# Kernel optimization log

Hardware: AMD Instinct MI355X
Metric: run time of the kernel (lower is better)

Reference implementation:

```python
import jax, jax.numpy as jnp
import numpy as np

N = 10000        # num_nodes
F_IN = 256       # dataset_num_features
H = 128          # hidden_channels
C_OUT = 40       # dataset_num_classes
L = 3            # num_layers
HEADS = 8
DH = H // HEADS  # per-head dim
E = 160000       # num edges (before self loops)
SCALE = 1.0 / float(np.sqrt(DH))


def setup_inputs() -> dict:
    key = jax.random.key(0)
    ks = jax.random.split(key, 8)
    s = lambda k, *sh: (jax.random.normal(k, sh, dtype=jnp.float32) * 0.05)
    return dict(
        edge_index=jax.random.randint(ks[0], (2, E), 0, N, dtype=jnp.int32),
        x_param=s(ks[1], N, F_IN),
        lin1_w=s(ks[2], F_IN, H),
        lin1_b=jnp.zeros((H,), jnp.float32),
        wq=s(ks[3], L, H, H),
        wk=s(ks[4], L, H, H),
        wv=s(ks[5], L, H, H),
        bq=jnp.zeros((L, H), jnp.float32),
        bk=jnp.zeros((L, H), jnp.float32),
        bv=jnp.zeros((L, H), jnp.float32),
        lin2_w=s(ks[6], H, C_OUT),
        lin2_b=jnp.zeros((C_OUT,), jnp.float32),
    )


def _gcn_norm(edge_index):
    # PyG gcn_norm: add self loops (weight 1), symmetric D^-1/2 A D^-1/2
    loops = jnp.arange(N, dtype=edge_index.dtype)
    row = jnp.concatenate([edge_index[0], loops])  # source j
    col = jnp.concatenate([edge_index[1], loops])  # target i
    deg = jax.ops.segment_sum(jnp.ones(row.shape, jnp.float32), col, num_segments=N)
    dis = jnp.where(deg > 0, jax.lax.rsqrt(jnp.maximum(deg, 1e-12)), 0.0)
    return row, col, dis[row] * dis[col]


def _restricted_softmax(score):
    # softmax with an implicit extra logit at `margin=0`
    m = jnp.maximum(jnp.max(score, axis=-1, keepdims=True), 0.0)
    e = jnp.exp(score - m)
    return e / (jnp.sum(e, axis=-1, keepdims=True) + jnp.exp(-m))


def _forward(edge_index, x_param, lin1_w, lin1_b, wq, wk, wv, bq, bk, bv, lin2_w, lin2_b):
    row, col, norm = _gcn_norm(edge_index)
    # dropouts are eval-mode no-ops
    x = jax.nn.relu(x_param @ lin1_w + lin1_b)  # [N, H]
    x_all = x[:, None, :]                       # [N, 1, H]
    for l in range(L):
        t = x_all.shape[1]
        # project per-node first (linear commutes with per-edge gather)
        q = (x_all[:, -1] @ wq[l] + bq[l]).reshape(N, HEADS, DH)      # query from latest state
        k = (x_all @ wk[l] + bk[l]).reshape(N, t, HEADS, DH)          # keys over full history
        v = (x_all @ wv[l] + bv[l]).reshape(N, t, HEADS, DH)
        qe = q[col]   # [Etot, heads, dh]   (x_i)
        ke = k[row]   # [Etot, t, heads, dh] (x_j)
        ve = v[row]
        score = jnp.einsum('ehd,ethd->eht', qe, ke) * SCALE
        attn = _restricted_softmax(score)        # attention-dropout is a no-op in eval
        msg = jnp.einsum('eht,ethd->ehd', attn, ve).reshape(-1, H) * norm[:, None]
        out = jax.ops.segment_sum(msg, col, num_segments=N)  # aggr='add'
        x = jax.nn.relu(out)
        x_all = jnp.concatenate([x_all, x[:, None, :]], axis=1)
    logits = x_all[:, -1] @ lin2_w + lin2_b
    return jax.nn.log_softmax(logits, axis=1)


def reference(edge_index, x_param, lin1_w, lin1_b, wq, wk, wv, bq, bk, bv, lin2_w, lin2_b):
    return _forward(edge_index, x_param, lin1_w, lin1_b, wq, wk, wv, bq, bk, bv, lin2_w, lin2_b)
```

## Files before the change

### kernel.cpp

```cpp
#include <hip/hip_runtime.h>
#include <math.h>

#define N_NODES 10000
#define F_IN_D  256
#define H_DIM   128
#define C_OUTD  40
#define NHEADS  8
#define NEDGES  160000
#define ETOT    (NEDGES + N_NODES)
#define SCALE_F 0.25f
#define TILES_N 157
#define KVSZ    ((size_t)N_NODES * 3 * 256)

typedef __attribute__((ext_vector_type(8))) short bf16x8;
typedef __attribute__((ext_vector_type(4))) float f32x4;
typedef __attribute__((ext_vector_type(2))) float f32x2;

__device__ __forceinline__ unsigned short f2bf(float f) {
    unsigned int u = __float_as_uint(f);
    unsigned int r = (u + 0x7FFFu + ((u >> 16) & 1u)) >> 16;
    return (unsigned short)r;
}
__device__ __forceinline__ float bf2f(unsigned short h) {
    return __uint_as_float(((unsigned int)h) << 16);
}
__device__ __forceinline__ unsigned char f2fp8(float v) {
    int pk = __builtin_amdgcn_cvt_pk_fp8_f32(v, v, 0, false);
    return (unsigned char)(pk & 0xff);
}


__global__ __launch_bounds__(256) void k_prep1(const float* __restrict__ w1,
                                               unsigned short* __restrict__ W1T,
                                               int* __restrict__ degi) {
    int t = blockIdx.x * 256 + threadIdx.x;
    if (t < 8192) {
        float4 v = *(const float4*)(w1 + 4 * t);
        int e = 4 * t;
        #pragma unroll
        for (int i = 0; i < 4; ++i) {
            int k = (e + i) >> 7, n = (e + i) & 127;
            W1T[n * 256 + k] = f2bf(((const float*)&v)[i]);
        }
    } else if (t < 10692) {
        int idx = (t - 8192) * 4;
        *(int4*)&degi[idx] = make_int4(0, 0, 0, 0);
    }
}


__device__ __forceinline__ void lin1_block(int bid, int ct0, const float* __restrict__ X,
                                           const unsigned short* __restrict__ W1T,
                                           const float* __restrict__ b1,
                                           unsigned short* __restrict__ X0, int nct) {
    int tid = threadIdx.x;
    int wid = tid >> 6, lane = tid & 63;
    int m = lane & 15, quad = lane >> 4;
    int rowA = bid * 64 + wid * 16 + m;
    int rowc = rowA < N_NODES ? rowA : N_NODES - 1;
    bf16x8 af[8];
    const float* ap = X + (size_t)rowc * F_IN_D + quad * 8;
    #pragma unroll
    for (int s = 0; s < 8; ++s) {
        float4 lo = *(const float4*)(ap + s * 32);
        float4 hi = *(const float4*)(ap + s * 32 + 4);
        union { unsigned short u[8]; bf16x8 v; } pk;
        pk.u[0] = f2bf(lo.x); pk.u[1] = f2bf(lo.y);
        pk.u[2] = f2bf(lo.z); pk.u[3] = f2bf(lo.w);
        pk.u[4] = f2bf(hi.x); pk.u[5] = f2bf(hi.y);
        pk.u[6] = f2bf(hi.z); pk.u[7] = f2bf(hi.w);
        af[s] = pk.v;
    }
    int row0 = bid * 64 + wid * 16 + quad * 4;
    for (int ct = ct0; ct < ct0 + nct; ++ct) {
        int col = ct * 16 + m;
        const unsigned short* bp = W1T + (size_t)col * F_IN_D + quad * 8;
        f32x4 acc = {0.f, 0.f, 0.f, 0.f};
        #pragma unroll
        for (int s = 0; s < 8; ++s) {
            bf16x8 bfr = __builtin_bit_cast(bf16x8, *(const uint4*)(bp + s * 32));
            acc = __builtin_amdgcn_mfma_f32_16x16x32_bf16(af[s], bfr, acc, 0, 0, 0);
        }
        float bb = b1[col];
        #pragma unroll
        for (int rg = 0; rg < 4; ++rg) {
            int r = row0 + rg;
            if (r < N_NODES)
                X0[(size_t)r * H_DIM + col] = f2bf(fmaxf(acc[rg] + bb, 0.f));
        }
    }
}

__device__ __forceinline__ void qkv_block(int mi, int rt,
                                          const unsigned short* __restrict__ XHb,
                                          const unsigned short* __restrict__ WTq_l,
                                          const unsigned short* __restrict__ WTk_l,
                                          const unsigned short* __restrict__ WTv_l,
                                          const float* __restrict__ bq_l,
                                          const float* __restrict__ bk_l,
                                          const float* __restrict__ bv_l,
                                          unsigned short* __restrict__ Qb,
                                          unsigned char* __restrict__ KVb,
                                          int hasQ, int qslice, int nK, int sbase,
                                          int cp0, int nct) {
    int tid = threadIdx.x;
    int wid = tid >> 6, lane = tid & 63;
    int m = lane & 15, quad = lane >> 4;
    const unsigned short* WT; const float* bias; int slice, mode;
    if (hasQ && mi == 0) { WT = WTq_l; bias = bq_l; slice = qslice; mode = 0; }
    else {
        int j = mi - hasQ;
        if (j < nK) { WT = WTk_l; bias = bk_l; slice = sbase + j;      mode = 1; }
        else        { WT = WTv_l; bias = bv_l; slice = sbase + j - nK; mode = 2; }
    }
    const unsigned short* A = XHb + (size_t)slice * N_NODES * H_DIM;
    int rowA = rt * 64 + wid * 16 + m;
    bf16x8 af[4];
    const unsigned short* ap = A + (size_t)rowA * H_DIM + quad * 8;
    #pragma unroll
    for (int s = 0; s < 4; ++s)
        af[s] = __builtin_bit_cast(bf16x8, *(const uint4*)(ap + s * 32));
    int row0 = rt * 64 + wid * 16 + quad * 4;
    int vofs = (mode == 2) ? 8 : 0;
    for (int cp = cp0; cp < cp0 + nct; ++cp) {
        int colA = cp * 32 + m;
        int colB = colA + 16;
        const unsigned short* bpA = WT + (size_t)colA * H_DIM + quad * 8;
        const unsigned short* bpB = WT + (size_t)colB * H_DIM + quad * 8;
        bf16x8 bA[4], bB[4];
        #pragma unroll
        for (int s = 0; s < 4; ++s) {
            bA[s] = __builtin_bit_cast(bf16x8, *(const uint4*)(bpA + s * 32));
            bB[s] = __builtin_bit_cast(bf16x8, *(const uint4*)(bpB + s * 32));
        }
        f32x4 accA = {0.f, 0.f, 0.f, 0.f};
        f32x4 accB = {0.f, 0.f, 0.f, 0.f};
        #pragma unroll
        for (int s = 0; s < 4; ++s) {
            accA = __builtin_amdgcn_mfma_f32_16x16x32_bf16(af[s], bA[s], accA, 0, 0, 0);
            accB = __builtin_amdgcn_mfma_f32_16x16x32_bf16(af[s], bB[s], accB, 0, 0, 0);
        }
        float bbA = bias[colA], bbB = bias[colB];
        #pragma unroll
        for (int rg = 0; rg < 4; ++rg) {
            int r = row0 + rg;
            if (r < N_NODES) {
                float vA = accA[rg] + bbA;
                float vB = accB[rg] + bbB;
                if (mode == 0) {
                    Qb[(size_t)r * H_DIM + colA] = f2bf(vA * SCALE_F);
                    Qb[(size_t)r * H_DIM + colB] = f2bf(vB * SCALE_F);
                } else {
                    size_t nb = ((size_t)r * 3 + slice) * 256;
                    KVb[nb + (colA >> 3) * 16 + (colA & 7) + vofs] = f2fp8(vA);
                    KVb[nb + (colB >> 3) * 16 + (colB & 7) + vofs] = f2fp8(vB);
                }
            }
        }
    }
}


template <int T>
__device__ __forceinline__ void kv_load(const uint4* __restrict__ KV, int r, int ci,
                                        uint4 (&kv)[T]) {
    const uint4* p = KV + (size_t)r * 48 + ci;
    #pragma unroll
    for (int s = 0; s < T; ++s) kv[s] = p[s * 16];
}

template <int T>
__device__ __forceinline__ void edge_accum(const uint4 (&kv)[T], const float (&q)[8],
                                           float nrm, float (&a)[8]) {
    float den = 1.f;
    float mv[8];
    #pragma unroll
    for (int i = 0; i < 8; ++i) mv[i] = 0.f;
    #pragma unroll
    for (int s = 0; s < T; ++s) {
        f32x2 k0 = __builtin_amdgcn_cvt_pk_f32_fp8(kv[s].x, false);
        f32x2 k1 = __builtin_amdgcn_cvt_pk_f32_fp8(kv[s].x, true);
        f32x2 k2 = __builtin_amdgcn_cvt_pk_f32_fp8(kv[s].y, false);
        f32x2 k3 = __builtin_amdgcn_cvt_pk_f32_fp8(kv[s].y, true);
        float p = q[0] * k0[0] + q[1] * k0[1] + q[2] * k1[0] + q[3] * k1[1]
                + q[4] * k2[0] + q[5] * k2[1] + q[6] * k3[0] + q[7] * k3[1];
        p += __shfl_xor(p, 1, 2);
        float w = __expf(p);
        den += w;
        f32x2 v0 = __builtin_amdgcn_cvt_pk_f32_fp8(kv[s].z, false);
        f32x2 v1 = __builtin_amdgcn_cvt_pk_f32_fp8(kv[s].z, true);
        f32x2 v2 = __builtin_amdgcn_cvt_pk_f32_fp8(kv[s].w, false);
        f32x2 v3 = __builtin_amdgcn_cvt_pk_f32_fp8(kv[s].w, true);
        mv[0] += w * v0[0]; mv[1] += w * v0[1];
        mv[2] += w * v1[0]; mv[3] += w * v1[1];
        mv[4] += w * v2[0]; mv[5] += w * v2[1];
        mv[6] += w * v3[0]; mv[7] += w * v3[1];
    }
    float ws = __fdividef(nrm, den);
    #pragma unroll
    for (int i = 0; i < 8; ++i) a[i] += ws * mv[i];
}

template <int T, bool LOGITS>
__device__ __forceinline__ void attn_block(int bid, const unsigned short* __restrict__ Q,
                                           const uint4* __restrict__ KV,
                                           const int2* __restrict__ csr,
                                           const int* __restrict__ degi,
                                           unsigned int* __restrict__ Xout,
                                           const unsigned short* __restrict__ W2T,
                                           const float* __restrict__ b2,
                                           float* __restrict__ out) {
    int tid = threadIdx.x;
    int wid = tid >> 6, lane = tid & 63;
    int quarter = lane >> 4, ci = lane & 15;
    int n = bid * 4 + wid;

    int cnt = degi[n] + 1;
    if (cnt > 64) cnt = 64;
    int li = lane < cnt ? lane : cnt - 1;
    int2 eAll = csr[(n << 6) + li];
    int   rAll = eAll.x;
    float nAll = (lane < cnt) ? __int_as_float(eAll.y) : 0.f;

    float q[8];
    {
        uint4 qp = *(const uint4*)&Q[(size_t)n * H_DIM + ci * 8];
        q[0] = __uint_as_float(qp.x << 16);
        q[1] = __uint_as_float(qp.x & 0xffff0000u);
        q[2] = __uint_as_float(qp.y << 16);
        q[3] = __uint_as_float(qp.y & 0xffff0000u);
        q[4] = __uint_as_float(qp.z << 16);
        q[5] = __uint_as_float(qp.z & 0xffff0000u);
        q[6] = __uint_as_float(qp.w << 16);
        q[7] = __uint_as_float(qp.w & 0xffff0000u);
    }
    int nq = (cnt + 3) >> 2;
    float a[8];
    #pragma unroll
    for (int i = 0; i < 8; ++i) a[i] = 0.f;

    auto rowN = [&](int j4) { return __shfl(rAll, j4 < 63 ? j4 : 63, 64); };
    auto nrmN = [&](int j4) { return __shfl(nAll, j4 < 63 ? j4 : 63, 64); };

    uint4 kv0[T], kv1[T], kv2[T], kv3[T];
    kv_load<T>(KV, rowN(quarter), ci, kv0);
    kv_load<T>(KV, rowN(4 + quarter), ci, kv1);
    kv_load<T>(KV, rowN(8 + quarter), ci, kv2);
    kv_load<T>(KV, rowN(12 + quarter), ci, kv3);

    int j = 0;
    for (;;) {
        edge_accum<T>(kv0, q, nrmN(j * 4 + quarter), a);
        if (++j >= nq) break;
        kv_load<T>(KV, rowN((j + 3) * 4 + quarter), ci, kv0);
        edge_accum<T>(kv1, q, nrmN(j * 4 + quarter), a);
        if (++j >= nq) break;
        kv_load<T>(KV, rowN((j + 3) * 4 + quarter), ci, kv1);
        edge_accum<T>(kv2, q, nrmN(j * 4 + quarter), a);
        if (++j >= nq) break;
        kv_load<T>(KV, rowN((j + 3) * 4 + quarter), ci, kv2);
        edge_accum<T>(kv3, q, nrmN(j * 4 + quarter), a);
        if (++j >= nq) break;
        kv_load<T>(KV, rowN((j + 3) * 4 + quarter), ci, kv3);
    }

    #pragma unroll
    for (int i = 0; i < 8; ++i) {
        a[i] += __shfl_xor(a[i], 16, 64);
        a[i] += __shfl_xor(a[i], 32, 64);
    }

    if (!LOGITS) {
        if (quarter == 0) {
            uint4 o;
            o.x = ((unsigned int)f2bf(fmaxf(a[1], 0.f)) << 16) | (unsigned int)f2bf(fmaxf(a[0], 0.f));
            o.y = ((unsigned int)f2bf(fmaxf(a[3], 0.f)) << 16) | (unsigned int)f2bf(fmaxf(a[2], 0.f));
            o.z = ((unsigned int)f2bf(fmaxf(a[5], 0.f)) << 16) | (unsigned int)f2bf(fmaxf(a[4], 0.f));
            o.w = ((unsigned int)f2bf(fmaxf(a[7], 0.f)) << 16) | (unsigned int)f2bf(fmaxf(a[6], 0.f));
            *(uint4*)&Xout[(size_t)n * 64 + ci * 4] = o;
        }
        return;
    }

    float x[8];
    #pragma unroll
    for (int i = 0; i < 8; ++i) x[i] = fmaxf(a[i], 0.f);
    float lg[10];
    #pragma unroll
    for (int jj = 0; jj < 10; ++jj) {
        int c = quarter * 10 + jj;
        uint4 w = *(const uint4*)&W2T[c * H_DIM + ci * 8];
        float p = x[0] * bf2f((unsigned short)(w.x & 0xffff))
                + x[1] * bf2f((unsigned short)(w.x >> 16))
                + x[2] * bf2f((unsigned short)(w.y & 0xffff))
                + x[3] * bf2f((unsigned short)(w.y >> 16))
                + x[4] * bf2f((unsigned short)(w.z & 0xffff))
                + x[5] * bf2f((unsigned short)(w.z >> 16))
                + x[6] * bf2f((unsigned short)(w.w & 0xffff))
                + x[7] * bf2f((unsigned short)(w.w >> 16));
        #pragma unroll
        for (int o = 1; o < 16; o <<= 1) p += __shfl_xor(p, o, 16);
        lg[jj] = p + b2[c];
    }
    float mx = lg[0];
    #pragma unroll
    for (int jj = 1; jj < 10; ++jj) mx = fmaxf(mx, lg[jj]);
    mx = fmaxf(mx, __shfl_xor(mx, 16, 64));
    mx = fmaxf(mx, __shfl_xor(mx, 32, 64));
    float sm = 0.f;
    #pragma unroll
    for (int jj = 0; jj < 10; ++jj) sm += __expf(lg[jj] - mx);
    sm += __shfl_xor(sm, 16, 64);
    sm += __shfl_xor(sm, 32, 64);
    float lse = mx + __logf(sm);
    if (ci == 0) {
        float* op = out + (size_t)n * C_OUTD + quarter * 10;
        #pragma unroll
        for (int jj = 0; jj < 10; ++jj) op[jj] = lg[jj] - lse;
    }
}


__global__ __launch_bounds__(256) void k_deg_lin1(const int* __restrict__ col,
                                                  int* __restrict__ degi,
                                                  int* __restrict__ slotbuf,
                                                  const float* __restrict__ X,
                                                  const unsigned short* __restrict__ W1T,
                                                  const float* __restrict__ b1,
                                                  unsigned short* __restrict__ X0,
                                                  const float* __restrict__ wq,
                                                  const float* __restrict__ wk,
                                                  const float* __restrict__ wv,
                                                  const float* __restrict__ w2,
                                                  unsigned short* __restrict__ WTq,
                                                  unsigned short* __restrict__ WTk,
                                                  unsigned short* __restrict__ WTv,
                                                  unsigned short* __restrict__ W2T,
                                                  int nct) {
    int b = blockIdx.x;
    if (b < 625) {
        int e = b * 256 + threadIdx.x;
        slotbuf[e] = atomicAdd(&degi[col[e]], 1);
        return;
    }
    if (b < 939) {
        int bid = b - 625;
        lin1_block(bid % TILES_N, (bid / TILES_N) * 4, X, W1T, b1, X0, nct);
        return;
    }
    int t = (b - 939) * 256 + threadIdx.x;
    if (t < 36864) {
        int mat = t >> 12;
        int l = mat / 3, ws = mat % 3;
        const float*    src = (ws == 0) ? wq  : (ws == 1) ? wk  : wv;
        unsigned short* dst = (ws == 0) ? WTq : (ws == 1) ? WTk : WTv;
        int e2 = (t & 4095) * 4;
        float4 v = *(const float4*)(src + l * 16384 + e2);
        #pragma unroll
        for (int i = 0; i < 4; ++i) {
            int k = (e2 + i) >> 7, n = (e2 + i) & 127;
            dst[l * 16384 + n * 128 + k] = f2bf(((const float*)&v)[i]);
        }
    } else if (t < 38144) {
        int e = (t - 36864) * 4;
        float4 v = *(const float4*)(w2 + e);
        #pragma unroll
        for (int i = 0; i < 4; ++i) {
            int ee = e + i;
            int k = ee / 40, c = ee - k * 40;
            W2T[c * H_DIM + k] = f2bf(((const float*)&v)[i]);
        }
    }
}

__global__ __launch_bounds__(256) void k_scatter_qkv0(const int* __restrict__ row,
                                                      const int* __restrict__ col,
                                                      const int* __restrict__ degi,
                                                      const int* __restrict__ slotbuf,
                                                      int2* __restrict__ csr,
                                                      const unsigned short* __restrict__ XHb,
                                                      const unsigned short* __restrict__ WTq,
                                                      const unsigned short* __restrict__ WTk,
                                                      const unsigned short* __restrict__ WTv,
                                                      const float* __restrict__ bq,
                                                      const float* __restrict__ bk,
                                                      const float* __restrict__ bv,
                                                      unsigned short* __restrict__ Qb,
                                                      unsigned char* __restrict__ KVb) {
    if (blockIdx.x < 665) {
        int e = blockIdx.x * 256 + threadIdx.x;
        if (e >= ETOT) return;
        int r, c, slot;
        if (e < NEDGES) { r = row[e]; c = col[e]; slot = slotbuf[e]; }
        else            { r = c = e - NEDGES; slot = degi[c]; }
        if (slot > 63) slot = 63;
        float dr = rsqrtf((float)(degi[r] + 1));
        float dc = rsqrtf((float)(degi[c] + 1));
        int2 ent; ent.x = r; ent.y = __float_as_int(dr * dc);
        csr[(c << 6) + slot] = ent;
        return;
    }
    int b = blockIdx.x - 665;
    int quarter = b / (3 * TILES_N);
    int bb = b % (3 * TILES_N);
    qkv_block(bb / TILES_N, bb % TILES_N, XHb, WTq, WTk, WTv, bq, bk, bv,
              Qb, KVb, 1, 0, 1, 0, quarter, 1);
}

__global__ __launch_bounds__(256) void k_attn0_old(const unsigned short* __restrict__ Q,
                                                   const uint4* __restrict__ KV,
                                                   const int2* __restrict__ csr,
                                                   const int* __restrict__ degi,
                                                   unsigned int* __restrict__ Xout,
                                                   const unsigned short* __restrict__ XHb,
                                                   const unsigned short* __restrict__ WTk,
                                                   const unsigned short* __restrict__ WTv,
                                                   const float* __restrict__ bk,
                                                   const float* __restrict__ bv,
                                                   unsigned char* __restrict__ B1,
                                                   unsigned char* __restrict__ B2) {
    if (blockIdx.x < 2500) {
        attn_block<1, false>(blockIdx.x, Q, KV, csr, degi, Xout,
                             nullptr, nullptr, nullptr);
        return;
    }
    int bb = blockIdx.x - 2500;
    int layer = bb / (2 * TILES_N);
    int r = bb % (2 * TILES_N);
    int mi = r / TILES_N;
    int rt = r % TILES_N;
    int woff = (layer + 1) * 16384;
    unsigned char* dst = layer ? B2 : B1;
    qkv_block(mi, rt, XHb, nullptr, WTk + woff, WTv + woff, nullptr,
              bk + (layer + 1) * H_DIM, bv + (layer + 1) * H_DIM, nullptr,
              dst, 0, 0, 1, 0, 0, 4);
}

__global__ __launch_bounds__(256) void k_qkvnew1_old2b(const unsigned short* __restrict__ XHb,
                                                       const unsigned short* __restrict__ WTq,
                                                       const unsigned short* __restrict__ WTk,
                                                       const unsigned short* __restrict__ WTv,
                                                       const float* __restrict__ bq,
                                                       const float* __restrict__ bk,
                                                       const float* __restrict__ bv,
                                                       unsigned short* __restrict__ Qb,
                                                       unsigned char* __restrict__ B1,
                                                       unsigned char* __restrict__ B2) {
    int b = blockIdx.x;
    if (b < 12 * TILES_N) {
        int quarter = b / (3 * TILES_N);
        int bb = b % (3 * TILES_N);
        qkv_block(bb / TILES_N, bb % TILES_N, XHb,
                  WTq + 16384, WTk + 16384, WTv + 16384,
                  bq + H_DIM, bk + H_DIM, bv + H_DIM,
                  Qb, B1, 1, 1, 1, 1, quarter, 1);
        return;
    }
    int b2 = b - 12 * TILES_N;
    int quarter = b2 / (2 * TILES_N);
    int bb = b2 % (2 * TILES_N);
    int mi = bb / TILES_N;
    qkv_block(mi, bb % TILES_N, XHb, nullptr, WTk + 32768, WTv + 32768, nullptr,
              bk + 2 * H_DIM, bv + 2 * H_DIM, nullptr,
              B2, 0, 0, 1, 1, quarter, 1);
}

template <int T>
__global__ __launch_bounds__(256) void k_attn_pure(const unsigned short* __restrict__ Q,
                                                   const uint4* __restrict__ KV,
                                                   const int2* __restrict__ csr,
                                                   const int* __restrict__ degi,
                                                   unsigned int* __restrict__ Xout) {
    attn_block<T, false>(blockIdx.x, Q, KV, csr, degi, Xout,
                         nullptr, nullptr, nullptr);
}

__global__ __launch_bounds__(256) void k_qkv2(const unsigned short* __restrict__ XHb,
                                              const unsigned short* __restrict__ WTq,
                                              const unsigned short* __restrict__ WTk,
                                              const unsigned short* __restrict__ WTv,
                                              const float* __restrict__ bq,
                                              const float* __restrict__ bk,
                                              const float* __restrict__ bv,
                                              unsigned short* __restrict__ Qb,
                                              unsigned char* __restrict__ B2) {
    int quarter = blockIdx.x / (3 * TILES_N);
    int bb = blockIdx.x % (3 * TILES_N);
    qkv_block(bb / TILES_N, bb % TILES_N, XHb,
              WTq + 32768, WTk + 32768, WTv + 32768,
              bq + 2 * H_DIM, bk + 2 * H_DIM, bv + 2 * H_DIM,
              Qb, B2, 1, 2, 1, 2, quarter, 1);
}

__global__ __launch_bounds__(256) void k_attn_logits(const unsigned short* __restrict__ Q,
                                                     const uint4* __restrict__ KV,
                                                     const int2* __restrict__ csr,
                                                     const int* __restrict__ degi,
                                                     const unsigned short* __restrict__ W2T,
                                                     const float* __restrict__ b2,
                                                     float* __restrict__ out) {
    attn_block<3, true>(blockIdx.x, Q, KV, csr, degi, nullptr, W2T, b2, out);
}


extern "C" void kernel_launch(void* const* d_in, const int* in_sizes, int n_in,
                              void* d_out, int out_size, void* d_ws, size_t ws_size,
                              hipStream_t stream) {
    const int*   ei      = (const int*)d_in[0];
    const int*   row     = ei;
    const int*   col     = ei + NEDGES;
    const float* x_param = (const float*)d_in[1];
    const float* lin1_w  = (const float*)d_in[2];
    const float* lin1_b  = (const float*)d_in[3];
    const float* wq      = (const float*)d_in[4];
    const float* wk      = (const float*)d_in[5];
    const float* wv      = (const float*)d_in[6];
    const float* bq      = (const float*)d_in[7];
    const float* bk      = (const float*)d_in[8];
    const float* bv      = (const float*)d_in[9];
    const float* lin2_w  = (const float*)d_in[10];
    const float* lin2_b  = (const float*)d_in[11];
    float*       out     = (float*)d_out;

    char* wbase = (char*)d_ws;
    size_t off = 0;
    auto alloc = [&](size_t bytes) -> void* {
        off = (off + 255) & ~(size_t)255;
        void* p = wbase + off;
        off += bytes;
        return p;
    };
    int*            degi     = (int*)           alloc((size_t)N_NODES * 4);
    int*            slotbuf  = (int*)           alloc((size_t)NEDGES * 4);
    int2*           csr      = (int2*)          alloc((size_t)N_NODES * 64 * 8);
    unsigned short* W1T      = (unsigned short*)alloc((size_t)H_DIM * F_IN_D * 2);
    unsigned short* WTq      = (unsigned short*)alloc((size_t)3 * H_DIM * H_DIM * 2);
    unsigned short* WTk      = (unsigned short*)alloc((size_t)3 * H_DIM * H_DIM * 2);
    unsigned short* WTv      = (unsigned short*)alloc((size_t)3 * H_DIM * H_DIM * 2);
    unsigned short* W2T      = (unsigned short*)alloc((size_t)C_OUTD * H_DIM * 2);
    unsigned short* XHb      = (unsigned short*)alloc((size_t)3 * N_NODES * H_DIM * 2);
    unsigned short* Qb       = (unsigned short*)alloc((size_t)N_NODES * H_DIM * 2);
    unsigned char*  KVb      = (unsigned char*) alloc(3 * KVSZ);
    unsigned char*  B0 = KVb;
    unsigned char*  B1 = KVb + KVSZ;
    unsigned char*  B2 = KVb + 2 * KVSZ;

    k_prep1<<<42, 256, 0, stream>>>(lin1_w, W1T, degi);

    k_deg_lin1<<<1089, 256, 0, stream>>>(col, degi, slotbuf,
                                         x_param, W1T, lin1_b, XHb,
                                         wq, wk, wv, lin2_w,
                                         WTq, WTk, WTv, W2T, 4);

    k_scatter_qkv0<<<665 + 12 * TILES_N, 256, 0, stream>>>(
        row, col, degi, slotbuf, csr,
        XHb, WTq, WTk, WTv, bq, bk, bv, Qb, B0);

    unsigned int* X1 = (unsigned int*)(XHb + (size_t)1 * N_NODES * H_DIM);
    unsigned int* X2 = (unsigned int*)(XHb + (size_t)2 * N_NODES * H_DIM);

    k_attn0_old<<<2500 + 4 * TILES_N, 256, 0, stream>>>(
        Qb, (const uint4*)B0, csr, degi, X1,
        XHb, WTk, WTv, bk, bv, B1, B2);

    k_qkvnew1_old2b<<<20 * TILES_N, 256, 0, stream>>>(
        XHb, WTq, WTk, WTv, bq, bk, bv, Qb, B1, B2);

    k_attn_pure<2><<<2500, 256, 0, stream>>>(Qb, (const uint4*)B1, csr, degi, X2);

    k_qkv2<<<12 * TILES_N, 256, 0, stream>>>(
        XHb, WTq, WTk, WTv, bq, bk, bv, Qb, B2);

    k_attn_logits<<<2500, 256, 0, stream>>>(Qb, (const uint4*)B2, csr, degi,
                                            W2T, lin2_b, out);
}
```

Measured before the change: 219.3 us.

## Fuse lin1 with layer-0 QKV projections via LDS and build CSR in one pass

Weight transposes are merged into a single prep kernel. lin1 output is kept in LDS and immediately projected to Q and to all K/V history slices for every layer, so X0 never goes to global memory. The CSR build now stores source ids directly through a single atomic pass, and edge norms are recomputed from degrees inside the attention kernels, which removes the slotbuf pass and halves the CSR entry size. The schedule drops from 8 launches to 7, at the cost of serial per-block projection work in the fused kernel and extra degree lookups during attention.

```diff
diff --git a/kernel.cpp b/kernel.cpp
--- a/kernel.cpp
+++ b/kernel.cpp
@@ -7,7 +7,6 @@
 #define C_OUTD  40
 #define NHEADS  8
 #define NEDGES  160000
-#define ETOT    (NEDGES + N_NODES)
 #define SCALE_F 0.25f
 #define TILES_N 157
 #define KVSZ    ((size_t)N_NODES * 3 * 256)
@@ -30,9 +29,17 @@
 }
 
 
-__global__ __launch_bounds__(256) void k_prep1(const float* __restrict__ w1,
-                                               unsigned short* __restrict__ W1T,
-                                               int* __restrict__ degi) {
+__global__ __launch_bounds__(256) void k_prep_all(const float* __restrict__ w1,
+                                                  const float* __restrict__ wq,
+                                                  const float* __restrict__ wk,
+                                                  const float* __restrict__ wv,
+                                                  const float* __restrict__ w2,
+                                                  unsigned short* __restrict__ W1T,
+                                                  unsigned short* __restrict__ WTq,
+                                                  unsigned short* __restrict__ WTk,
+                                                  unsigned short* __restrict__ WTv,
+                                                  unsigned short* __restrict__ W2T,
+                                                  int* __restrict__ degi) {
     int t = blockIdx.x * 256 + threadIdx.x;
     if (t < 8192) {
         float4 v = *(const float4*)(w1 + 4 * t);
@@ -42,86 +49,44 @@
             int k = (e + i) >> 7, n = (e + i) & 127;
             W1T[n * 256 + k] = f2bf(((const float*)&v)[i]);
         }
-    } else if (t < 10692) {
-        int idx = (t - 8192) * 4;
+    } else if (t < 45056) {
+        int u = t - 8192;
+        int mat = u >> 12;
+        int l = mat / 3, ws = mat % 3;
+        const float*    src = (ws == 0) ? wq  : (ws == 1) ? wk  : wv;
+        unsigned short* dst = (ws == 0) ? WTq : (ws == 1) ? WTk : WTv;
+        int e2 = (u & 4095) * 4;
+        float4 v = *(const float4*)(src + l * 16384 + e2);
+        #pragma unroll
+        for (int i = 0; i < 4; ++i) {
+            int k = (e2 + i) >> 7, n = (e2 + i) & 127;
+            dst[l * 16384 + n * 128 + k] = f2bf(((const float*)&v)[i]);
+        }
+    } else if (t < 46336) {
+        int e = (t - 45056) * 4;
+        float4 v = *(const float4*)(w2 + e);
+        #pragma unroll
+        for (int i = 0; i < 4; ++i) {
+            int ee = e + i;
+            int k = ee / 40, c = ee - k * 40;
+            W2T[c * H_DIM + k] = f2bf(((const float*)&v)[i]);
+        }
+    } else if (t < 48836) {
+        int idx = (t - 46336) * 4;
         *(int4*)&degi[idx] = make_int4(0, 0, 0, 0);
     }
 }
 
 
-__device__ __forceinline__ void lin1_block(int bid, int ct0, const float* __restrict__ X,
-                                           const unsigned short* __restrict__ W1T,
-                                           const float* __restrict__ b1,
-                                           unsigned short* __restrict__ X0, int nct) {
-    int tid = threadIdx.x;
-    int wid = tid >> 6, lane = tid & 63;
-    int m = lane & 15, quad = lane >> 4;
-    int rowA = bid * 64 + wid * 16 + m;
-    int rowc = rowA < N_NODES ? rowA : N_NODES - 1;
-    bf16x8 af[8];
-    const float* ap = X + (size_t)rowc * F_IN_D + quad * 8;
-    #pragma unroll
-    for (int s = 0; s < 8; ++s) {
-        float4 lo = *(const float4*)(ap + s * 32);
-        float4 hi = *(const float4*)(ap + s * 32 + 4);
-        union { unsigned short u[8]; bf16x8 v; } pk;
-        pk.u[0] = f2bf(lo.x); pk.u[1] = f2bf(lo.y);
-        pk.u[2] = f2bf(lo.z); pk.u[3] = f2bf(lo.w);
-        pk.u[4] = f2bf(hi.x); pk.u[5] = f2bf(hi.y);
-        pk.u[6] = f2bf(hi.z); pk.u[7] = f2bf(hi.w);
-        af[s] = pk.v;
-    }
-    int row0 = bid * 64 + wid * 16 + quad * 4;
-    for (int ct = ct0; ct < ct0 + nct; ++ct) {
-        int col = ct * 16 + m;
-        const unsigned short* bp = W1T + (size_t)col * F_IN_D + quad * 8;
-        f32x4 acc = {0.f, 0.f, 0.f, 0.f};
-        #pragma unroll
-        for (int s = 0; s < 8; ++s) {
-            bf16x8 bfr = __builtin_bit_cast(bf16x8, *(const uint4*)(bp + s * 32));
-            acc = __builtin_amdgcn_mfma_f32_16x16x32_bf16(af[s], bfr, acc, 0, 0, 0);
-        }
-        float bb = b1[col];
-        #pragma unroll
-        for (int rg = 0; rg < 4; ++rg) {
-            int r = row0 + rg;
-            if (r < N_NODES)
-                X0[(size_t)r * H_DIM + col] = f2bf(fmaxf(acc[rg] + bb, 0.f));
-        }
-    }
-}
-
-__device__ __forceinline__ void qkv_block(int mi, int rt,
-                                          const unsigned short* __restrict__ XHb,
-                                          const unsigned short* __restrict__ WTq_l,
-                                          const unsigned short* __restrict__ WTk_l,
-                                          const unsigned short* __restrict__ WTv_l,
-                                          const float* __restrict__ bq_l,
-                                          const float* __restrict__ bk_l,
-                                          const float* __restrict__ bv_l,
-                                          unsigned short* __restrict__ Qb,
-                                          unsigned char* __restrict__ KVb,
-                                          int hasQ, int qslice, int nK, int sbase,
-                                          int cp0, int nct) {
-    int tid = threadIdx.x;
-    int wid = tid >> 6, lane = tid & 63;
-    int m = lane & 15, quad = lane >> 4;
-    const unsigned short* WT; const float* bias; int slice, mode;
-    if (hasQ && mi == 0) { WT = WTq_l; bias = bq_l; slice = qslice; mode = 0; }
-    else {
-        int j = mi - hasQ;
-        if (j < nK) { WT = WTk_l; bias = bk_l; slice = sbase + j;      mode = 1; }
-        else        { WT = WTv_l; bias = bv_l; slice = sbase + j - nK; mode = 2; }
-    }
-    const unsigned short* A = XHb + (size_t)slice * N_NODES * H_DIM;
-    int rowA = rt * 64 + wid * 16 + m;
-    bf16x8 af[4];
-    const unsigned short* ap = A + (size_t)rowA * H_DIM + quad * 8;
-    #pragma unroll
-    for (int s = 0; s < 4; ++s)
-        af[s] = __builtin_bit_cast(bf16x8, *(const uint4*)(ap + s * 32));
-    int row0 = rt * 64 + wid * 16 + quad * 4;
+__device__ __forceinline__ void proj_frags(const bf16x8 (&af)[4], int row0, int m,
+                                           int quad,
+                                           const unsigned short* __restrict__ WT,
+                                           const float* __restrict__ bias, int mode,
+                                           unsigned short* __restrict__ Qb,
+                                           unsigned char* __restrict__ KVbuf,
+                                           int kvslice, int cp0, int nct) {
     int vofs = (mode == 2) ? 8 : 0;
+    #pragma unroll 1
     for (int cp = cp0; cp < cp0 + nct; ++cp) {
         int colA = cp * 32 + m;
         int colB = colA + 16;
@@ -151,13 +116,118 @@
                     Qb[(size_t)r * H_DIM + colA] = f2bf(vA * SCALE_F);
                     Qb[(size_t)r * H_DIM + colB] = f2bf(vB * SCALE_F);
                 } else {
-                    size_t nb = ((size_t)r * 3 + slice) * 256;
-                    KVb[nb + (colA >> 3) * 16 + (colA & 7) + vofs] = f2fp8(vA);
-                    KVb[nb + (colB >> 3) * 16 + (colB & 7) + vofs] = f2fp8(vB);
+                    size_t nb = ((size_t)r * 3 + kvslice) * 256;
+                    KVbuf[nb + (colA >> 3) * 16 + (colA & 7) + vofs] = f2fp8(vA);
+                    KVbuf[nb + (colB >> 3) * 16 + (colB & 7) + vofs] = f2fp8(vB);
                 }
             }
         }
     }
+}
+
+__device__ __forceinline__ void qkv_mat(int mode, int rt,
+                                        const unsigned short* __restrict__ A,
+                                        const unsigned short* __restrict__ WT,
+                                        const float* __restrict__ bias,
+                                        unsigned short* __restrict__ Qb,
+                                        unsigned char* __restrict__ KVbuf,
+                                        int kvslice, int cp0, int nct) {
+    int tid = threadIdx.x;
+    int wid = tid >> 6, lane = tid & 63;
+    int m = lane & 15, quad = lane >> 4;
+    int rowA = rt * 64 + wid * 16 + m;
+    bf16x8 af[4];
+    const unsigned short* ap = A + (size_t)rowA * H_DIM + quad * 8;
+    #pragma unroll
+    for (int s = 0; s < 4; ++s)
+        af[s] = __builtin_bit_cast(bf16x8, *(const uint4*)(ap + s * 32));
+    int row0 = rt * 64 + wid * 16 + quad * 4;
+    proj_frags(af, row0, m, quad, WT, bias, mode, Qb, KVbuf, kvslice, cp0, nct);
+}
+
+
+#define LDS_W 136
+
+__global__ __launch_bounds__(256) void k_fused0(const float* __restrict__ X,
+                                                const unsigned short* __restrict__ W1T,
+                                                const float* __restrict__ b1,
+                                                const int* __restrict__ erow,
+                                                const int* __restrict__ ecol,
+                                                int* __restrict__ degi,
+                                                int* __restrict__ csr,
+                                                const unsigned short* __restrict__ WTq,
+                                                const unsigned short* __restrict__ WTk,
+                                                const unsigned short* __restrict__ WTv,
+                                                const float* __restrict__ bq,
+                                                const float* __restrict__ bk,
+                                                const float* __restrict__ bv,
+                                                unsigned short* __restrict__ Qb,
+                                                unsigned char* __restrict__ B0,
+                                                unsigned char* __restrict__ B1,
+                                                unsigned char* __restrict__ B2,
+                                                int nct) {
+    __shared__ unsigned short xl[64][LDS_W];
+    if (blockIdx.x >= TILES_N) {
+        int e = (blockIdx.x - TILES_N) * 256 + threadIdx.x;
+        int c = ecol[e];
+        int slot = atomicAdd(&degi[c], 1);
+        if (slot < 64) csr[(c << 6) + slot] = erow[e];
+        return;
+    }
+    int rt = blockIdx.x;
+    int tid = threadIdx.x;
+    int wid = tid >> 6, lane = tid & 63;
+    int m = lane & 15, quad = lane >> 4;
+
+    {
+        int rowA = rt * 64 + wid * 16 + m;
+        int rowc = rowA < N_NODES ? rowA : N_NODES - 1;
+        bf16x8 af8[8];
+        const float* ap = X + (size_t)rowc * F_IN_D + quad * 8;
+        #pragma unroll
+        for (int s = 0; s < 8; ++s) {
+            float4 lo = *(const float4*)(ap + s * 32);
+            float4 hi = *(const float4*)(ap + s * 32 + 4);
+            union { unsigned short u[8]; bf16x8 v; } pk;
+            pk.u[0] = f2bf(lo.x); pk.u[1] = f2bf(lo.y);
+            pk.u[2] = f2bf(lo.z); pk.u[3] = f2bf(lo.w);
+            pk.u[4] = f2bf(hi.x); pk.u[5] = f2bf(hi.y);
+            pk.u[6] = f2bf(hi.z); pk.u[7] = f2bf(hi.w);
+            af8[s] = pk.v;
+        }
+        #pragma unroll 1
+        for (int ct = 0; ct < 2 * nct; ++ct) {
+            int col = ct * 16 + m;
+            const unsigned short* bp = W1T + (size_t)col * F_IN_D + quad * 8;
+            f32x4 acc = {0.f, 0.f, 0.f, 0.f};
+            #pragma unroll
+            for (int s = 0; s < 8; ++s) {
+                bf16x8 bfr = __builtin_bit_cast(bf16x8, *(const uint4*)(bp + s * 32));
+                acc = __builtin_amdgcn_mfma_f32_16x16x32_bf16(af8[s], bfr, acc, 0, 0, 0);
+            }
+            float bb = b1[col];
+            #pragma unroll
+            for (int rg = 0; rg < 4; ++rg)
+                xl[wid * 16 + quad * 4 + rg][col] = f2bf(fmaxf(acc[rg] + bb, 0.f));
+        }
+    }
+    __syncthreads();
+
+    bf16x8 af[4];
+    {
+        int rl = wid * 16 + m;
+        #pragma unroll
+        for (int s = 0; s < 4; ++s)
+            af[s] = *(const bf16x8*)&xl[rl][quad * 8 + s * 32];
+    }
+    int row0 = rt * 64 + wid * 16 + quad * 4;
+    proj_frags(af, row0, m, quad, WTq,         bq,             0, Qb, nullptr, 0, 0, nct);
+    proj_frags(af, row0, m, quad, WTk,         bk,             1, nullptr, B0, 0, 0, nct);
+    proj_frags(af, row0, m, quad, WTv,         bv,             2, nullptr, B0, 0, 0, nct);
+    proj_frags(af, row0, m, quad, WTk + 16384, bk + H_DIM,     1, nullptr, B1, 0, 0, nct);
+    proj_frags(af, row0, m, quad, WTv + 16384, bv + H_DIM,     2, nullptr, B1, 0, 0, nct);
+    proj_frags(af, row0, m, quad, WTk + 32768, bk + 2 * H_DIM, 1, nullptr, B2, 0, 0, nct);
+    proj_frags(af, row0, m, quad, WTv + 32768, bv + 2 * H_DIM, 2, nullptr, B2, 0, 0, nct);
 }
 
 
@@ -204,7 +274,7 @@
 template <int T, bool LOGITS>
 __device__ __forceinline__ void attn_block(int bid, const unsigned short* __restrict__ Q,
                                            const uint4* __restrict__ KV,
-                                           const int2* __restrict__ csr,
+                                           const int* __restrict__ csr,
                                            const int* __restrict__ degi,
                                            unsigned int* __restrict__ Xout,
                                            const unsigned short* __restrict__ W2T,
@@ -215,12 +285,15 @@
     int quarter = lane >> 4, ci = lane & 15;
     int n = bid * 4 + wid;
 
-    int cnt = degi[n] + 1;
+    int dn = degi[n];
+    int cnt = dn + 1;
     if (cnt > 64) cnt = 64;
-    int li = lane < cnt ? lane : cnt - 1;
-    int2 eAll = csr[(n << 6) + li];
-    int   rAll = eAll.x;
-    float nAll = (lane < cnt) ? __int_as_float(eAll.y) : 0.f;
+    float rn = rsqrtf((float)(dn + 1));
+    int csrv = csr[(n << 6) + lane];
+    int r = (lane < cnt - 1) ? csrv : n;
+    int dr = degi[r];
+    int   rAll = r;
+    float nAll = (lane < cnt) ? rsqrtf((float)(dr + 1)) * rn : 0.f;
 
     float q[8];
     {
@@ -321,161 +394,17 @@
 }
 
 
-__global__ __launch_bounds__(256) void k_deg_lin1(const int* __restrict__ col,
-                                                  int* __restrict__ degi,
-                                                  int* __restrict__ slotbuf,
-                                                  const float* __restrict__ X,
-                                                  const unsigned short* __restrict__ W1T,
-                                                  const float* __restrict__ b1,
-                                                  unsigned short* __restrict__ X0,
-                                                  const float* __restrict__ wq,
-                                                  const float* __restrict__ wk,
-                                                  const float* __restrict__ wv,
-                                                  const float* __restrict__ w2,
-                                                  unsigned short* __restrict__ WTq,
-                                                  unsigned short* __restrict__ WTk,
-                                                  unsigned short* __restrict__ WTv,
-                                                  unsigned short* __restrict__ W2T,
-                                                  int nct) {
-    int b = blockIdx.x;
-    if (b < 625) {
-        int e = b * 256 + threadIdx.x;
-        slotbuf[e] = atomicAdd(&degi[col[e]], 1);
-        return;
-    }
-    if (b < 939) {
-        int bid = b - 625;
-        lin1_block(bid % TILES_N, (bid / TILES_N) * 4, X, W1T, b1, X0, nct);
-        return;
-    }
-    int t = (b - 939) * 256 + threadIdx.x;
-    if (t < 36864) {
-        int mat = t >> 12;
-        int l = mat / 3, ws = mat % 3;
-        const float*    src = (ws == 0) ? wq  : (ws == 1) ? wk  : wv;
-        unsigned short* dst = (ws == 0) ? WTq : (ws == 1) ? WTk : WTv;
-        int e2 = (t & 4095) * 4;
-        float4 v = *(const float4*)(src + l * 16384 + e2);
-        #pragma unroll
-        for (int i = 0; i < 4; ++i) {
-            int k = (e2 + i) >> 7, n = (e2 + i) & 127;
-            dst[l * 16384 + n * 128 + k] = f2bf(((const float*)&v)[i]);
-        }
-    } else if (t < 38144) {
-        int e = (t - 36864) * 4;
-        float4 v = *(const float4*)(w2 + e);
-        #pragma unroll
-        for (int i = 0; i < 4; ++i) {
-            int ee = e + i;
-            int k = ee / 40, c = ee - k * 40;
-            W2T[c * H_DIM + k] = f2bf(((const float*)&v)[i]);
-        }
-    }
-}
-
-__global__ __launch_bounds__(256) void k_scatter_qkv0(const int* __restrict__ row,
-                                                      const int* __restrict__ col,
-                                                      const int* __restrict__ degi,
-                                                      const int* __restrict__ slotbuf,
-                                                      int2* __restrict__ csr,
-                                                      const unsigned short* __restrict__ XHb,
-                                                      const unsigned short* __restrict__ WTq,
-                                                      const unsigned short* __restrict__ WTk,
-                                                      const unsigned short* __restrict__ WTv,
-                                                      const float* __restrict__ bq,
-                                                      const float* __restrict__ bk,
-                                                      const float* __restrict__ bv,
-                                                      unsigned short* __restrict__ Qb,
-                                                      unsigned char* __restrict__ KVb) {
-    if (blockIdx.x < 665) {
-        int e = blockIdx.x * 256 + threadIdx.x;
-        if (e >= ETOT) return;
-        int r, c, slot;
-        if (e < NEDGES) { r = row[e]; c = col[e]; slot = slotbuf[e]; }
-        else            { r = c = e - NEDGES; slot = degi[c]; }
-        if (slot > 63) slot = 63;
-        float dr = rsqrtf((float)(degi[r] + 1));
-        float dc = rsqrtf((float)(degi[c] + 1));
-        int2 ent; ent.x = r; ent.y = __float_as_int(dr * dc);
-        csr[(c << 6) + slot] = ent;
-        return;
-    }
-    int b = blockIdx.x - 665;
-    int quarter = b / (3 * TILES_N);
-    int bb = b % (3 * TILES_N);
-    qkv_block(bb / TILES_N, bb % TILES_N, XHb, WTq, WTk, WTv, bq, bk, bv,
-              Qb, KVb, 1, 0, 1, 0, quarter, 1);
-}
-
-__global__ __launch_bounds__(256) void k_attn0_old(const unsigned short* __restrict__ Q,
-                                                   const uint4* __restrict__ KV,
-                                                   const int2* __restrict__ csr,
-                                                   const int* __restrict__ degi,
-                                                   unsigned int* __restrict__ Xout,
-                                                   const unsigned short* __restrict__ XHb,
-                                                   const unsigned short* __restrict__ WTk,
-                                                   const unsigned short* __restrict__ WTv,
-                                                   const float* __restrict__ bk,
-                                                   const float* __restrict__ bv,
-                                                   unsigned char* __restrict__ B1,
-                                                   unsigned char* __restrict__ B2) {
-    if (blockIdx.x < 2500) {
-        attn_block<1, false>(blockIdx.x, Q, KV, csr, degi, Xout,
-                             nullptr, nullptr, nullptr);
-        return;
-    }
-    int bb = blockIdx.x - 2500;
-    int layer = bb / (2 * TILES_N);
-    int r = bb % (2 * TILES_N);
-    int mi = r / TILES_N;
-    int rt = r % TILES_N;
-    int woff = (layer + 1) * 16384;
-    unsigned char* dst = layer ? B2 : B1;
-    qkv_block(mi, rt, XHb, nullptr, WTk + woff, WTv + woff, nullptr,
-              bk + (layer + 1) * H_DIM, bv + (layer + 1) * H_DIM, nullptr,
-              dst, 0, 0, 1, 0, 0, 4);
-}
-
-__global__ __launch_bounds__(256) void k_qkvnew1_old2b(const unsigned short* __restrict__ XHb,
-                                                       const unsigned short* __restrict__ WTq,
-                                                       const unsigned short* __restrict__ WTk,
-                                                       const unsigned short* __restrict__ WTv,
-                                                       const float* __restrict__ bq,
-                                                       const float* __restrict__ bk,
-                                                       const float* __restrict__ bv,
-                                                       unsigned short* __restrict__ Qb,
-                                                       unsigned char* __restrict__ B1,
-                                                       unsigned char* __restrict__ B2) {
-    int b = blockIdx.x;
-    if (b < 12 * TILES_N) {
-        int quarter = b / (3 * TILES_N);
-        int bb = b % (3 * TILES_N);
-        qkv_block(bb / TILES_N, bb % TILES_N, XHb,
-                  WTq + 16384, WTk + 16384, WTv + 16384,
-                  bq + H_DIM, bk + H_DIM, bv + H_DIM,
-                  Qb, B1, 1, 1, 1, 1, quarter, 1);
-        return;
-    }
-    int b2 = b - 12 * TILES_N;
-    int quarter = b2 / (2 * TILES_N);
-    int bb = b2 % (2 * TILES_N);
-    int mi = bb / TILES_N;
-    qkv_block(mi, bb % TILES_N, XHb, nullptr, WTk + 32768, WTv + 32768, nullptr,
-              bk + 2 * H_DIM, bv + 2 * H_DIM, nullptr,
-              B2, 0, 0, 1, 1, quarter, 1);
-}
-
 template <int T>
 __global__ __launch_bounds__(256) void k_attn_pure(const unsigned short* __restrict__ Q,
                                                    const uint4* __restrict__ KV,
-                                                   const int2* __restrict__ csr,
+                                                   const int* __restrict__ csr,
                                                    const int* __restrict__ degi,
                                                    unsigned int* __restrict__ Xout) {
     attn_block<T, false>(blockIdx.x, Q, KV, csr, degi, Xout,
                          nullptr, nullptr, nullptr);
 }
 
-__global__ __launch_bounds__(256) void k_qkv2(const unsigned short* __restrict__ XHb,
+__global__ __launch_bounds__(256) void k_qkv5(const unsigned short* __restrict__ X1,
                                               const unsigned short* __restrict__ WTq,
                                               const unsigned short* __restrict__ WTk,
                                               const unsigned short* __restrict__ WTv,
@@ -483,18 +412,48 @@
                                               const float* __restrict__ bk,
                                               const float* __restrict__ bv,
                                               unsigned short* __restrict__ Qb,
-                                              unsigned char* __restrict__ B2) {
-    int quarter = blockIdx.x / (3 * TILES_N);
-    int bb = blockIdx.x % (3 * TILES_N);
-    qkv_block(bb / TILES_N, bb % TILES_N, XHb,
-              WTq + 32768, WTk + 32768, WTv + 32768,
-              bq + 2 * H_DIM, bk + 2 * H_DIM, bv + 2 * H_DIM,
-              Qb, B2, 1, 2, 1, 2, quarter, 1);
+                                              unsigned char* __restrict__ B1,
+                                              unsigned char* __restrict__ B2,
+                                              int nct) {
+    int b = blockIdx.x;
+    int split = b / (5 * TILES_N);
+    int r = b % (5 * TILES_N);
+    int mat = r / TILES_N, rt = r % TILES_N;
+    int cp0 = split * 2;
+    switch (mat) {
+    case 0: qkv_mat(0, rt, X1, WTq + 16384, bq + H_DIM,     Qb, nullptr, 0, cp0, nct); break;
+    case 1: qkv_mat(1, rt, X1, WTk + 16384, bk + H_DIM,     nullptr, B1, 1, cp0, nct); break;
+    case 2: qkv_mat(2, rt, X1, WTv + 16384, bv + H_DIM,     nullptr, B1, 1, cp0, nct); break;
+    case 3: qkv_mat(1, rt, X1, WTk + 32768, bk + 2 * H_DIM, nullptr, B2, 1, cp0, nct); break;
+    default: qkv_mat(2, rt, X1, WTv + 32768, bv + 2 * H_DIM, nullptr, B2, 1, cp0, nct); break;
+    }
+}
+
+__global__ __launch_bounds__(256) void k_qkv3(const unsigned short* __restrict__ X2,
+                                              const unsigned short* __restrict__ WTq,
+                                              const unsigned short* __restrict__ WTk,
+                                              const unsigned short* __restrict__ WTv,
+                                              const float* __restrict__ bq,
+                                              const float* __restrict__ bk,
+                                              const float* __restrict__ bv,
+                                              unsigned short* __restrict__ Qb,
+                                              unsigned char* __restrict__ B2,
+                                              int nct) {
+    int b = blockIdx.x;
+    int split = b / (3 * TILES_N);
+    int r = b % (3 * TILES_N);
+    int mat = r / TILES_N, rt = r % TILES_N;
+    int cp0 = split * 2;
+    switch (mat) {
+    case 0: qkv_mat(0, rt, X2, WTq + 32768, bq + 2 * H_DIM, Qb, nullptr, 0, cp0, nct); break;
+    case 1: qkv_mat(1, rt, X2, WTk + 32768, bk + 2 * H_DIM, nullptr, B2, 2, cp0, nct); break;
+    default: qkv_mat(2, rt, X2, WTv + 32768, bv + 2 * H_DIM, nullptr, B2, 2, cp0, nct); break;
+    }
 }
 
 __global__ __launch_bounds__(256) void k_attn_logits(const unsigned short* __restrict__ Q,
                                                      const uint4* __restrict__ KV,
-                                                     const int2* __restrict__ csr,
+                                                     const int* __restrict__ csr,
                                                      const int* __restrict__ degi,
                                                      const unsigned short* __restrict__ W2T,
                                                      const float* __restrict__ b2,
@@ -531,45 +490,40 @@
         return p;
     };
     int*            degi     = (int*)           alloc((size_t)N_NODES * 4);
-    int*            slotbuf  = (int*)           alloc((size_t)NEDGES * 4);
-    int2*           csr      = (int2*)          alloc((size_t)N_NODES * 64 * 8);
+    int*            csr      = (int*)           alloc((size_t)N_NODES * 64 * 4);
     unsigned short* W1T      = (unsigned short*)alloc((size_t)H_DIM * F_IN_D * 2);
     unsigned short* WTq      = (unsigned short*)alloc((size_t)3 * H_DIM * H_DIM * 2);
     unsigned short* WTk      = (unsigned short*)alloc((size_t)3 * H_DIM * H_DIM * 2);
     unsigned short* WTv      = (unsigned short*)alloc((size_t)3 * H_DIM * H_DIM * 2);
     unsigned short* W2T      = (unsigned short*)alloc((size_t)C_OUTD * H_DIM * 2);
-    unsigned short* XHb      = (unsigned short*)alloc((size_t)3 * N_NODES * H_DIM * 2);
+    unsigned short* XHb      = (unsigned short*)alloc((size_t)2 * N_NODES * H_DIM * 2);
     unsigned short* Qb       = (unsigned short*)alloc((size_t)N_NODES * H_DIM * 2);
     unsigned char*  KVb      = (unsigned char*) alloc(3 * KVSZ);
     unsigned char*  B0 = KVb;
     unsigned char*  B1 = KVb + KVSZ;
     unsigned char*  B2 = KVb + 2 * KVSZ;
 
-    k_prep1<<<42, 256, 0, stream>>>(lin1_w, W1T, degi);
-
-    k_deg_lin1<<<1089, 256, 0, stream>>>(col, degi, slotbuf,
-                                         x_param, W1T, lin1_b, XHb,
-                                         wq, wk, wv, lin2_w,
-                                         WTq, WTk, WTv, W2T, 4);
-
-    k_scatter_qkv0<<<665 + 12 * TILES_N, 256, 0, stream>>>(
-        row, col, degi, slotbuf, csr,
-        XHb, WTq, WTk, WTv, bq, bk, bv, Qb, B0);
-
-    unsigned int* X1 = (unsigned int*)(XHb + (size_t)1 * N_NODES * H_DIM);
-    unsigned int* X2 = (unsigned int*)(XHb + (size_t)2 * N_NODES * H_DIM);
-
-    k_attn0_old<<<2500 + 4 * TILES_N, 256, 0, stream>>>(
-        Qb, (const uint4*)B0, csr, degi, X1,
-        XHb, WTk, WTv, bk, bv, B1, B2);
-
-    k_qkvnew1_old2b<<<20 * TILES_N, 256, 0, stream>>>(
-        XHb, WTq, WTk, WTv, bq, bk, bv, Qb, B1, B2);
-
-    k_attn_pure<2><<<2500, 256, 0, stream>>>(Qb, (const uint4*)B1, csr, degi, X2);
-
-    k_qkv2<<<12 * TILES_N, 256, 0, stream>>>(
-        XHb, WTq, WTk, WTv, bq, bk, bv, Qb, B2);
+    k_prep_all<<<191, 256, 0, stream>>>(lin1_w, wq, wk, wv, lin2_w,
+                                        W1T, WTq, WTk, WTv, W2T, degi);
+
+    k_fused0<<<TILES_N + 625, 256, 0, stream>>>(
+        x_param, W1T, lin1_b, row, col, degi, csr,
+        WTq, WTk, WTv, bq, bk, bv, Qb, B0, B1, B2, 4);
+
+    const unsigned short* X1 = XHb;
+    const unsigned short* X2 = XHb + (size_t)N_NODES * H_DIM;
+    unsigned int* X1w = (unsigned int*)XHb;
+    unsigned int* X2w = (unsigned int*)(XHb + (size_t)N_NODES * H_DIM);
+
+    k_attn_pure<1><<<2500, 256, 0, stream>>>(Qb, (const uint4*)B0, csr, degi, X1w);
+
+    k_qkv5<<<10 * TILES_N, 256, 0, stream>>>(X1, WTq, WTk, WTv, bq, bk, bv,
+                                             Qb, B1, B2, 2);
+
+    k_attn_pure<2><<<2500, 256, 0, stream>>>(Qb, (const uint4*)B1, csr, degi, X2w);
+
+    k_qkv3<<<6 * TILES_N, 256, 0, stream>>>(X2, WTq, WTk, WTv, bq, bk, bv,
+                                            Qb, B2, 2);
 
     k_attn_logits<<<2500, 256, 0, stream>>>(Qb, (const uint4*)B2, csr, degi,
                                             W2T, lin2_b, out);
```

New measurement: 240.5 us. +9.7%, slower.
